# Performance work log

Hardware: AMD Instinct MI355X
Metric: run time of the kernel (lower is better)

Reference implementation:

```python
import jax, jax.numpy as jnp
import numpy as np

B, M, F_IN, DX, K, L, N_ALL = 8192, 10, 128, 128, 64, 32, 100000
NN = M - 1          # n_neigh
INF = float(M)


def layer_norm(x, g, b, eps=1e-5):
    mu = x.mean(-1, keepdims=True)
    var = ((x - mu) ** 2).mean(-1, keepdims=True)
    return (x - mu) * jax.lax.rsqrt(var + eps) * g + b


def bfs_dists(adj, mask):
    # normalized all-pairs hop distances via repeated boolean matmul (m=10 fixed)
    adj_bin = (adj > 1e-5).astype(jnp.float32)
    eye = jnp.eye(M, dtype=bool)
    d = jnp.where(eye[None], 0.0, jnp.where(adj_bin > 0, 1.0, INF))
    curr = adj_bin
    for k in range(2, M):
        curr = jnp.matmul(curr, adj_bin)
        d = jnp.where((curr > 0) & (d == INF), float(k), d)
    mask2 = mask[:, :, None] * mask[:, None, :]
    d = jnp.where(mask2 == 0, INF, d)
    return d / float(M)


def compute_sw(zb, zp, theta, vmask):
    # sliced Wasserstein-2 between batch point clouds [B,NN,d] and prototypes [K,NN,d]
    tn = theta / jnp.linalg.norm(theta, axis=1, keepdims=True)
    pb = jnp.einsum('bmd,ld->bml', zb, tn)
    pp = jnp.einsum('kmd,ld->kml', zp, tn)
    idx = jnp.argsort(pb, axis=1)
    pbs = jnp.take_along_axis(pb, idx, axis=1)
    pps = jnp.sort(pp, axis=1)
    w = jnp.take_along_axis(jnp.broadcast_to(vmask[:, :, None], pb.shape), idx, axis=1)
    w = w / (w.sum(axis=1, keepdims=True) + 1e-9)
    # sum_m w*(pb-pp)^2 expanded to avoid materializing [B,K,NN,L]
    t1 = (w * pbs ** 2).sum(axis=1)                   # [B,L]
    t2 = jnp.einsum('bml,kml->bkl', w * pbs, pps)     # [B,K,L]
    t3 = jnp.einsum('bml,kml->bkl', w, pps ** 2)
    return (t1[:, None, :] - 2.0 * t2 + t3).mean(axis=-1)


def compute_radial(rb, rp, vmask):
    idx = jnp.argsort(rb, axis=1)
    rbs = jnp.take_along_axis(rb, idx, axis=1)
    rps = jnp.sort(rp, axis=1)
    w = jnp.take_along_axis(vmask, idx, axis=1)
    w = w / (w.sum(axis=1, keepdims=True) + 1e-9)
    return (((rbs[:, None, :] - rps[None]) ** 2) * w[:, None, :]).sum(-1)


def setup_inputs() -> dict:
    key = jax.random.key(0)
    ks = jax.random.split(key, 16)
    up = (jax.random.uniform(ks[0], (B, M, M)) < 0.3).astype(jnp.float32)
    adj = jnp.maximum(up, up.transpose(0, 2, 1)) * (1.0 - jnp.eye(M))
    features = jax.random.normal(ks[1], (N_ALL, F_IN), jnp.float32)
    idxs = jax.random.randint(ks[2], (B, M), 0, N_ALL + 1)   # N_ALL == padding index
    rn = lambda k, s, sc=0.02: sc * jax.random.normal(k, s, jnp.float32)
    params = dict(
        x_lin_w=rn(ks[3], (F_IN, DX), 0.05), x_lin_b=jnp.zeros((DX,)),
        x_ln_g=jnp.ones((DX,)), x_ln_b=jnp.zeros((DX,)),
        s_ln_g=jnp.ones((NN,)), s_ln_b=jnp.zeros((NN,)),
        theta_x=jax.random.normal(ks[4], (L, DX), jnp.float32),
        theta_s=jax.random.normal(ks[5], (L, NN), jnp.float32),
        alpha_raw=jnp.zeros(()),
        an_w1=rn(ks[6], (DX, 32), 0.1), an_b1=jnp.zeros((32,)),
        an_w2=rn(ks[7], (32, 1), 0.1), an_b2=jnp.zeros((1,)),
        wn_w1=rn(ks[8], (2 * DX, 32), 0.1), wn_b1=jnp.zeros((32,)),
        wn_w2=rn(ks[9], (32, 1), 0.1), wn_b2=jnp.zeros((1,)),
        w_raw=jnp.zeros(()),
        proto_root=jax.random.normal(ks[10], (K, F_IN), jnp.float32),
        proto_neigh=jax.random.normal(ks[11], (K, NN, F_IN), jnp.float32),
        proto_rad=jax.random.uniform(ks[12], (K, NN)),
        proto_dn=jax.random.uniform(ks[13], (NN * (NN - 1) // 2, K), minval=-0.5, maxval=0.5),
        log_gamma=jnp.asarray(np.log(0.01), jnp.float32),
    )
    return {"adj": adj, "features": features, "idxs": idxs, **params}


def reference(adj, features, idxs, x_lin_w, x_lin_b, x_ln_g, x_ln_b, s_ln_g, s_ln_b,
              theta_x, theta_s, alpha_raw, an_w1, an_b1, an_w2, an_b2,
              wn_w1, wn_b1, wn_w2, wn_b2, w_raw,
              proto_root, proto_neigh, proto_rad, proto_dn, log_gamma):
    b = adj.shape[0]
    x_all = jnp.concatenate([features, jnp.zeros((1, F_IN), features.dtype)], 0)
    x_patch = x_all[idxs]                             # [B,M,F]
    x_root, x_neigh = x_patch[:, 0], x_patch[:, 1:]
    vmask = (idxs[:, 1:] != N_ALL).astype(jnp.float32)   # [B,NN]
    lin = lambda x: x @ x_lin_w + x_lin_b
    h_root = layer_norm(lin(x_root), x_ln_g, x_ln_b)
    h_proto_root = layer_norm(lin(proto_root), x_ln_g, x_ln_b)
    d_root_feat = (jnp.sum(h_root ** 2, -1)[:, None] + jnp.sum(h_proto_root ** 2, -1)[None]
                   - 2.0 * h_root @ h_proto_root.T)   # squared cdist [B,K]
    full_mask = jnp.concatenate([jnp.ones((b, 1), jnp.float32), vmask], 1)
    dists_full = bfs_dists(adj, full_mask)
    d_radial_str = compute_radial(dists_full[:, 0, 1:], proto_rad, vmask)
    h_neigh = layer_norm(lin(x_neigh), x_ln_g, x_ln_b)     # dropout = identity (eval)
    h_proto_neigh = layer_norm(lin(proto_neigh), x_ln_g, x_ln_b)
    sw_neigh_feat = compute_sw(h_neigh, h_proto_neigh, theta_x, vmask)
    hs_neigh = layer_norm(jnp.sort(dists_full[:, 1:, 1:], axis=1), s_ln_g, s_ln_b)
    ti, tj = np.triu_indices(NN, 1)
    C = jnp.zeros((K, NN, NN)).at[:, ti, tj].set(jax.nn.sigmoid(proto_dn).T)
    C = C + C.transpose(0, 2, 1)
    hs_proto = layer_norm(jnp.sort(C, axis=1), s_ln_g, s_ln_b)
    sw_neigh_str = compute_sw(hs_neigh, hs_proto, theta_s, vmask)
    h_pooled = (h_neigh * vmask[:, :, None]).sum(1) / (vmask.sum(1, keepdims=True) + 1e-9)
    alpha_logit = jnp.maximum(h_pooled @ an_w1 + an_b1, 0.0) @ an_w2 + an_b2   # [B,1]
    alpha = jax.nn.sigmoid(alpha_raw + alpha_logit)
    # pairwise w_net([h_root; h_proto_root]) without materializing [B,K,2*DX]
    hb = h_root @ wn_w1[:DX] + wn_b1                   # [B,32]
    hp = h_proto_root @ wn_w1[DX:]                     # [K,32]
    w_logit = (jnp.maximum(hb[:, None] + hp[None], 0.0) @ wn_w2)[..., 0] + wn_b2[0]
    w = jax.nn.sigmoid(w_raw + w_logit)                # [B,K]
    d_feat = w * d_root_feat + (1.0 - w) * sw_neigh_feat
    d_str = w * d_radial_str + (1.0 - w) * sw_neigh_str
    d_fgw = alpha * d_feat + (1.0 - alpha) * d_str
    return jnp.exp(-jnp.exp(log_gamma) * d_fgw)        # [B,K]
```

## Files before the change

### kernel.cpp

```cpp
#include <hip/hip_runtime.h>
#include <hip/hip_bf16.h>

typedef unsigned short u16;
typedef __attribute__((ext_vector_type(8))) short short8;
typedef __attribute__((ext_vector_type(4))) float f32x4;

#define NN 9
#define DX 128
#define KP 64
#define LL 32
#define NALL 100000
#define BMAX 8192
#define NBM 16
#define NBP 64

#define MFMA(a, b, c) __builtin_amdgcn_mfma_f32_16x16x32_bf16(a, b, c, 0, 0, 0)
#define WFENCE() __threadfence_block()

__device__ __align__(16) float g_tns[LL * NN];
__device__ __align__(16) float g_hprn[KP];
__device__ __align__(16) float g_hpt[32 * KP];
__device__ __align__(16) float g_rpst[NN * KP];
__device__ __align__(16) u16   g_hx[BMAX * 10 * DX];
__device__ __align__(16) u16   g_hpool[BMAX * DX];
__device__ __align__(16) float g_hrn[BMAX];
__device__ __align__(16) u16   g_pW[16384];
__device__ __align__(16) u16   g_pBt[4096];
__device__ __align__(16) u16   g_pBr[8192];
__device__ __align__(16) u16   g_pBx[36864];
__device__ __align__(16) u16   g_pBs[36864];
__device__ __align__(16) u16   g_pAn[4096];
__device__ __align__(16) u16   g_pWn[4096];

__device__ __forceinline__ float bf2f(u16 u) {
    union { unsigned u; float f; } v; v.u = ((unsigned)u) << 16; return v.f;
}
__device__ __forceinline__ u16 f2bf(float f) {
    __hip_bfloat16 h = __float2bfloat16(f);
    union { __hip_bfloat16 h; u16 u; } v; v.h = h; return v.u;
}
__device__ __forceinline__ float ldv(const void* p, long i, int f32) {
    return f32 ? ((const float*)p)[i] : bf2f(((const u16*)p)[i]);
}
__device__ __forceinline__ float sigmoidf(float x) { return 1.f / (1.f + expf(-x)); }

__device__ __forceinline__ int bfrag_idx(int ksteps, int ncol, int kd) {
    int ntile = ncol >> 4, n = ncol & 15;
    int kstep = kd >> 5, quad = (kd >> 3) & 3, j = kd & 7;
    return ((ntile * ksteps + kstep) * 64 + quad * 16 + n) * 8 + j;
}

__device__ __forceinline__ void rank9(const float* v, int* r) {
#pragma unroll
    for (int m = 0; m < 9; m++) {
        int rk = 0;
#pragma unroll
        for (int n = 0; n < 9; n++)
            rk += (v[n] < v[m]) || (v[n] == v[m] && n < m);
        r[m] = rk;
    }
}

__global__ __launch_bounds__(256) void k_pack(
    const void* xlw, const void* theta_x, const void* theta_s,
    const void* an_w1, const void* wn_w1, const void* xlg) {
    int t = threadIdx.x;
    const int f32 = (((const u16*)xlg)[0] == 0);
    if (blockIdx.x == 0) {
        for (int i = t; i < 16384; i += 256) {
            int c = i >> 7, d = i & 127;
            g_pW[bfrag_idx(4, d, c)] = f2bf(ldv(xlw, i, f32));
        }
    } else if (blockIdx.x == 1) {
        if (t < 32) {
            float s = 0;
            for (int d = 0; d < 128; d++) { float v = ldv(theta_x, t * 128 + d, f32); s = fmaf(v, v, s); }
            float inv = 1.f / sqrtf(s);
            for (int d = 0; d < 128; d++)
                g_pBt[bfrag_idx(4, t, d)] = f2bf(ldv(theta_x, t * 128 + d, f32) * inv);
        } else if (t < 64) {
            int l = t - 32;
            float s = 0;
            for (int j = 0; j < 9; j++) { float v = ldv(theta_s, l * 9 + j, f32); s = fmaf(v, v, s); }
            float inv = 1.f / sqrtf(s);
            for (int j = 0; j < 9; j++) g_tns[l * 9 + j] = ldv(theta_s, l * 9 + j, f32) * inv;
        }
    } else {
        for (int i = t; i < 4096; i += 256) {
            int d = i >> 5, j = i & 31;
            g_pAn[bfrag_idx(4, j, d)] = f2bf(ldv(an_w1, i, f32));
            g_pWn[bfrag_idx(4, j, d)] = f2bf(ldv(wn_w1, i, f32));
        }
    }
}

__global__ __launch_bounds__(256, 4) void k_lin(
    const void* feat, const int* idxs,
    const void* proto_root, const void* proto_neigh,
    const void* xlb, const void* xlg, const void* xlbt,
    const void* slg, const void* slb, const void* wn_w1,
    const void* proto_rad, const void* proto_dn, int B) {
    __shared__ __align__(16) u16   WfL[16384];
    __shared__ __align__(16) u16   hXpb[1280];
    __shared__ __align__(16) float pbX[288];
    __shared__ __align__(16) float Cm[84];
    __shared__ __align__(16) float hsnP[84];
    u16* hS = WfL;

    int t = threadIdx.x, lane = t & 63, w = t >> 6;
    const int f32 = (((const u16*)xlg)[0] == 0);
    int fm = lane & 15, quad = lane >> 4;
    bool isProto = (blockIdx.x < (unsigned)NBP);
    int rcap = isProto ? 10 : 60;
    int base = isProto ? blockIdx.x * 10 : (blockIdx.x - NBP) * 60;
    int rowT = isProto ? KP * 10 : B * 10;

    {
        const short8* src = (const short8*)g_pW;
        short8* dst = (short8*)WfL;
#pragma unroll
        for (int i = 0; i < 8; i++) dst[t + 256 * i] = src[t + 256 * i];
    }

    int lr = w * 16 + fm, gr = base + lr;
    bool azero = true;
    const void* abuf = feat; long aoff = 0;
    if (lr < rcap && gr < rowT) {
        if (!isProto) {
            int id = idxs[gr];
            if (id != NALL) { azero = false; aoff = (long)id * 128; }
        } else {
            int rr = gr % 10; azero = false;
            if (rr < 9) { abuf = proto_neigh; aoff = (long)((gr / 10) * 9 + rr) * 128; }
            else        { abuf = proto_root;  aoff = (long)(gr / 10) * 128; }
        }
    }
    short8 af[4];
#pragma unroll
    for (int ks = 0; ks < 4; ks++) af[ks] = (short8){0, 0, 0, 0, 0, 0, 0, 0};
    if (!azero) {
        if (f32) {
#pragma unroll
            for (int ks = 0; ks < 4; ks++) {
                const f32x4* src = (const f32x4*)((const float*)abuf + aoff + ks * 32 + quad * 8);
                f32x4 v0 = src[0], v1 = src[1];
                u16* ap = (u16*)&af[ks];
#pragma unroll
                for (int j = 0; j < 4; j++) { ap[j] = f2bf(v0[j]); ap[4 + j] = f2bf(v1[j]); }
            }
        } else {
#pragma unroll
            for (int ks = 0; ks < 4; ks++)
                af[ks] = *(const short8*)((const u16*)abuf + aoff + ks * 32 + quad * 8);
        }
    }
    float bias8[8], gg8[8], bb8[8];
#pragma unroll
    for (int nt = 0; nt < 8; nt++) {
        int col = nt * 16 + fm;
        bias8[nt] = ldv(xlb, col, f32);
        gg8[nt]   = ldv(xlg, col, f32);
        bb8[nt]   = ldv(xlbt, col, f32);
    }
    __syncthreads();

    f32x4 acc[8];
#pragma unroll
    for (int nt = 0; nt < 8; nt++) acc[nt] = (f32x4){0.f, 0.f, 0.f, 0.f};
    if (w * 16 < rcap) {
#pragma unroll
        for (int ks = 0; ks < 4; ks++) {
#pragma unroll
            for (int nt = 0; nt < 8; nt++) {
                short8 bf = *(const short8*)(WfL + ((nt * 4 + ks) * 64 + lane) * 8);
                acc[nt] = MFMA(af[ks], bf, acc[nt]);
            }
        }
    }
    __syncthreads();

    if (w * 16 < rcap) {
#pragma unroll
        for (int reg = 0; reg < 4; reg++) {
            float s = 0, q = 0;
#pragma unroll
            for (int nt = 0; nt < 8; nt++) {
                float v = acc[nt][reg] + bias8[nt];
                s += v; q = fmaf(v, v, q);
            }
#pragma unroll
            for (int m = 1; m < 16; m <<= 1) { s += __shfl_xor(s, m); q += __shfl_xor(q, m); }
            float mu = s * (1.f / 128.f);
            float var = fmaxf(q * (1.f / 128.f) - mu * mu, 0.f);
            float rs = rsqrtf(var + 1e-5f);
            int rowD = w * 16 + quad * 4 + reg, grD = base + rowD;
            if (rowD < rcap && grD < rowT) {
#pragma unroll
                for (int nt = 0; nt < 8; nt++) {
                    float val = (acc[nt][reg] + bias8[nt] - mu) * rs * gg8[nt] + bb8[nt];
                    if (!isProto) hS[rowD * 128 + nt * 16 + fm] = f2bf(val);
                    else          hXpb[rowD * 128 + nt * 16 + fm] = f2bf(val);
                }
            }
        }
    }
    __syncthreads();

    if (!isProto) {
        int nrows = rowT - base; if (nrows > 60) nrows = 60;
        {
            const short8* src = (const short8*)hS;
            short8* dst = (short8*)(g_hx + (long)base * 128);
            for (int i = t; i < nrows * 16; i += 256) dst[i] = src[i];
        }
        if (t < 192) {
            int b = t >> 5, l = t & 31;
            int bg = base / 10 + b;
            if (b * 10 < nrows && bg < B) {
                unsigned msk9 = 0; int cnt = 0;
#pragma unroll
                for (int m = 0; m < 9; m++) {
                    if (idxs[bg * 10 + 1 + m] != NALL) { msk9 |= 1u << m; cnt++; }
                }
                float invb = 1.f / ((float)cnt + 1e-9f);
                float rq = 0;
                unsigned r01, r23;
                {
                    u16 o[4];
#pragma unroll
                    for (int cc = 0; cc < 4; cc++) {
                        int c = l * 4 + cc;
                        float a = 0;
#pragma unroll
                        for (int m = 0; m < 9; m++)
                            if ((msk9 >> m) & 1) a += bf2f(hS[(b * 10 + 1 + m) * 128 + c]);
                        o[cc] = f2bf(a * invb);
                        float rv = bf2f(hS[(b * 10) * 128 + c]);
                        rq = fmaf(rv, rv, rq);
                    }
                    r01 = (unsigned)o[0] | ((unsigned)o[1] << 16);
                    r23 = (unsigned)o[2] | ((unsigned)o[3] << 16);
                }
                unsigned* gp = (unsigned*)(g_hpool + (long)bg * 128);
                gp[l * 2]     = r01;
                gp[l * 2 + 1] = r23;
#pragma unroll
                for (int m = 16; m >= 1; m >>= 1) rq += __shfl_xor(rq, m);
                if (l == 0) g_hrn[bg] = rq;
            }
        }
        return;
    }

    int kb = blockIdx.x;

    for (int i = t; i < 128; i += 256)
        g_pBr[bfrag_idx(4, kb, i)] = hXpb[1152 + i];
    if (w == 0) {
        float v0 = bf2f(hXpb[1152 + lane]);
        float v1 = bf2f(hXpb[1216 + lane]);
        float q = v0 * v0 + v1 * v1;
#pragma unroll
        for (int m = 32; m >= 1; m >>= 1) q += __shfl_xor(q, m);
        if (lane == 0) g_hprn[kb] = q;
    }
    {
        int j = t >> 3, sub = t & 7;
        float a = 0;
#pragma unroll
        for (int dd = 0; dd < 16; dd++) {
            int d = sub * 16 + dd;
            a = fmaf(bf2f(hXpb[1152 + d]), ldv(wn_w1, (128 + d) * 32 + j, f32), a);
        }
        a += __shfl_xor(a, 1);
        a += __shfl_xor(a, 2);
        a += __shfl_xor(a, 4);
        if (sub == 0) g_hpt[j * 64 + kb] = a;
    }
    if (t == 0) {
        float v[9]; int r[9];
#pragma unroll
        for (int m = 0; m < 9; m++) v[m] = ldv(proto_rad, kb * 9 + m, f32);
        rank9(v, r);
#pragma unroll
        for (int m = 0; m < 9; m++) g_rpst[r[m] * 64 + kb] = v[m];
    }
    if (w == 0) {
        f32x4 acc0 = {0.f, 0.f, 0.f, 0.f}, acc1 = {0.f, 0.f, 0.f, 0.f};
        const u16* arow2 = hXpb + fm * 128;
#pragma unroll
        for (int ks = 0; ks < 4; ks++) {
            short8 afp = {0, 0, 0, 0, 0, 0, 0, 0};
            if (fm < 9) afp = *(const short8*)(arow2 + ks * 32 + quad * 8);
            short8 b0 = *(const short8*)(g_pBt + ((0 * 4 + ks) * 64 + lane) * 8);
            short8 b1 = *(const short8*)(g_pBt + ((1 * 4 + ks) * 64 + lane) * 8);
            acc0 = MFMA(afp, b0, acc0);
            acc1 = MFMA(afp, b1, acc1);
        }
#pragma unroll
        for (int reg = 0; reg < 4; reg++) {
            int row = quad * 4 + reg;
            if (row < 9) {
                pbX[row * 32 + fm]      = acc0[reg];
                pbX[row * 32 + 16 + fm] = acc1[reg];
            }
        }
    }
    for (int i = t; i < 81; i += 256) {
        int ii = i / 9, jj = i % 9; float v = 0.f;
        if (ii != jj) {
            int a = (ii < jj) ? ii : jj, b2 = (ii < jj) ? jj : ii;
            int p = a * 8 - a * (a - 1) / 2 + (b2 - a - 1);
            v = sigmoidf(ldv(proto_dn, p * 64 + kb, f32));
        }
        Cm[i] = v;
    }
    __syncthreads();
    if (t < 32) {
        float v[9]; int r[9];
#pragma unroll
        for (int m = 0; m < 9; m++) v[m] = pbX[m * 32 + t];
        rank9(v, r);
#pragma unroll
        for (int m = 0; m < 9; m++) {
            int kd = t * 9 + r[m];
            g_pBx[bfrag_idx(18, kb, kd)]       = f2bf(v[m] * v[m]);
            g_pBx[bfrag_idx(18, kb, 288 + kd)] = f2bf(v[m]);
        }
    }
    if (t >= 64 && t < 73) {
        int col = t - 64;
        float v[9]; int r[9];
#pragma unroll
        for (int j = 0; j < 9; j++) v[j] = Cm[j * 9 + col];
        rank9(v, r);
#pragma unroll
        for (int j = 0; j < 9; j++) Cm[r[j] * 9 + col] = v[j];
    }
    __syncthreads();
    if (t < 9) {
        float mu = 0;
#pragma unroll
        for (int j = 0; j < 9; j++) mu += Cm[t * 9 + j];
        mu *= (1.f / 9.f);
        float var = 0;
#pragma unroll
        for (int j = 0; j < 9; j++) { float d0 = Cm[t * 9 + j] - mu; var = fmaf(d0, d0, var); }
        var *= (1.f / 9.f);
        float rs = rsqrtf(var + 1e-5f);
#pragma unroll
        for (int j = 0; j < 9; j++)
            hsnP[t * 9 + j] = (Cm[t * 9 + j] - mu) * rs * ldv(slg, j, f32) + ldv(slb, j, f32);
    }
    __syncthreads();
    if (t < 32) {
#pragma unroll
        for (int m = 0; m < 9; m++) {
            float a = 0;
#pragma unroll
            for (int j = 0; j < 9; j++) a = fmaf(hsnP[m * 9 + j], g_tns[t * 9 + j], a);
            pbX[m * 32 + t] = a;
        }
    }
    __syncthreads();
    if (t < 32) {
        float v[9]; int r[9];
#pragma unroll
        for (int m = 0; m < 9; m++) v[m] = pbX[m * 32 + t];
        rank9(v, r);
#pragma unroll
        for (int m = 0; m < 9; m++) {
            int kd = t * 9 + r[m];
            g_pBs[bfrag_idx(18, kb, kd)]       = f2bf(v[m] * v[m]);
            g_pBs[bfrag_idx(18, kb, 288 + kd)] = f2bf(v[m]);
        }
    }
}

struct M3 {
    u16   Cf[NBM][584];
    u16   Cs[NBM][584];
    u16   hpoolb[NBM][136];
    float pb[NBM][288];
    float df[NBM][100];
    float hst[NBM][81];
    float drad[NBM][65];
    float hbv[NBM][33];
    float rbss[NBM][9], wrad[NBM][9];
    float sc[NBM][9];
};
__global__ __launch_bounds__(1024, 8) void k_main(
    const void* adj, const int* idxs,
    const void* slg, const void* slb,
    const void* an_b1, const void* an_w2, const void* an_b2,
    const void* wn_b1, const void* wn_w2, const void* wn_b2,
    const void* alpha_raw, const void* w_raw, const void* log_gamma,
    const void* xlg, void* out, int B) {
    __shared__ __align__(16) M3 S;
    int t = threadIdx.x, lane = t & 63, w = t >> 6;
    const int f32 = (((const u16*)xlg)[0] == 0);
    int fm = lane & 15, quad = lane >> 4;
    int bw = blockIdx.x * NBM + w;
    bool bv = (bw < B);

    unsigned long long mb = 0; float nv = 1e-9f, inv = 0.f;

    if (bv) {
        bool valid = false;
        if (lane < 10) {
            int id = idxs[bw * 10 + lane];
            valid = (lane == 0) || (id != NALL);
        }
        mb = __ballot(valid);
        nv = (float)__popcll(mb & 0x3FEull) + 1e-9f;
        inv = 1.f / nv;
        unsigned rowbits = 0;
        if (lane < 10) {
            for (int j = 0; j < 10; j++)
                if (ldv(adj, (long)bw * 100 + lane * 10 + j, f32) > 1e-5f) rowbits |= 1u << j;
        }
        int dl[10];
#pragma unroll
        for (int j = 0; j < 10; j++) dl[j] = (j == lane) ? 0 : (((rowbits >> j) & 1) ? 1 : 10);
        unsigned reach = (lane < 10) ? (rowbits | (1u << lane)) : 0u;
        for (int s = 2; s <= 9; s++) {
            unsigned nr = reach;
#pragma unroll
            for (int j = 0; j < 10; j++) {
                unsigned rj = __shfl(rowbits, j);
                if ((reach >> j) & 1) nr |= rj;
            }
            unsigned add = nr & ~reach;
#pragma unroll
            for (int j = 0; j < 10; j++) if ((add >> j) & 1) dl[j] = s;
            reach = nr;
            if (__all(add == 0)) break;
        }
        if (lane < 10) {
            int mi = (int)((mb >> lane) & 1);
#pragma unroll
            for (int j = 0; j < 10; j++) {
                int mj = (int)((mb >> j) & 1);
                S.df[w][lane * 10 + j] = (mi && mj) ? (float)dl[j] * 0.1f : 1.0f;
            }
        }
        {
            float v[9];
#pragma unroll
            for (int m = 0; m < 9; m++) {
                float vm = ((mb >> (1 + m)) & 1) ? (float)dl[1 + m] * 0.1f : 1.0f;
                v[m] = __shfl(vm, 0);
            }
            if (lane < 9) {
                float mine = v[0];
#pragma unroll
                for (int m = 1; m < 9; m++) if (lane == m) mine = v[m];
                int rk = 0;
#pragma unroll
                for (int n = 0; n < 9; n++) rk += (v[n] < mine) || (v[n] == mine && n < lane);
                S.rbss[w][rk] = mine;
                S.wrad[w][rk] = (((mb >> (1 + lane)) & 1) ? 1.f : 0.f) * inv;
            }
        }
        if (lane == 0) S.sc[w][1] = g_hrn[bw];
        ((unsigned*)S.hpoolb[w])[lane] = ((const unsigned*)(g_hpool + (long)bw * 128))[lane];
        {
            f32x4 acc0 = {0.f, 0.f, 0.f, 0.f}, acc1 = {0.f, 0.f, 0.f, 0.f};
            const u16* arow = g_hx + (bw * 10 + 1 + fm) * 128;
#pragma unroll
            for (int ks = 0; ks < 4; ks++) {
                short8 af = {0, 0, 0, 0, 0, 0, 0, 0};
                if (fm < 9) af = *(const short8*)(arow + ks * 32 + quad * 8);
                short8 b0 = *(const short8*)(g_pBt + ((0 * 4 + ks) * 64 + lane) * 8);
                short8 b1 = *(const short8*)(g_pBt + ((1 * 4 + ks) * 64 + lane) * 8);
                acc0 = MFMA(af, b0, acc0);
                acc1 = MFMA(af, b1, acc1);
            }
#pragma unroll
            for (int reg = 0; reg < 4; reg++) {
                int row = quad * 4 + reg;
                if (row < 9) {
                    S.pb[w][row * 32 + fm]      = acc0[reg];
                    S.pb[w][row * 32 + 16 + fm] = acc1[reg];
                }
            }
        }
        WFENCE();

        {
            float t1 = 0;
            if (lane < 32) {
                float v[9]; int r[9];
#pragma unroll
                for (int m = 0; m < 9; m++) v[m] = S.pb[w][m * 32 + lane];
                rank9(v, r);
#pragma unroll
                for (int m = 0; m < 9; m++) {
                    float wgt = (((mb >> (1 + m)) & 1) ? 1.f : 0.f) * inv;
                    int slot = lane * 9 + r[m];
                    S.Cf[w][slot]       = f2bf(wgt);
                    S.Cf[w][288 + slot] = f2bf(-2.f * wgt * v[m]);
                    t1 = fmaf(wgt * v[m], v[m], t1);
                }
            }
#pragma unroll
            for (int m = 16; m >= 1; m >>= 1) t1 += __shfl_xor(t1, m);
            if (lane == 0) S.sc[w][3] = t1;
        }
        if (lane < 9) {
            float v[9]; int r[9];
#pragma unroll
            for (int i = 0; i < 9; i++) v[i] = S.df[w][(1 + i) * 10 + 1 + lane];
            rank9(v, r);
#pragma unroll
            for (int i = 0; i < 9; i++) S.hst[w][r[i] * 9 + lane] = v[i];
        }
        {
            float acc = 0;
#pragma unroll
            for (int m = 0; m < 9; m++) {
                float d0 = S.rbss[w][m] - g_rpst[m * 64 + lane];
                acc = fmaf(d0 * d0, S.wrad[w][m], acc);
            }
            S.drad[w][lane] = acc;
        }
        WFENCE();

        if (lane < 9) {
            float vv[9];
#pragma unroll
            for (int j = 0; j < 9; j++) vv[j] = S.hst[w][lane * 9 + j];
            float mu = 0;
#pragma unroll
            for (int j = 0; j < 9; j++) mu += vv[j];
            mu *= (1.f / 9.f);
            float var = 0;
#pragma unroll
            for (int j = 0; j < 9; j++) { float d0 = vv[j] - mu; var = fmaf(d0, d0, var); }
            var *= (1.f / 9.f);
            float rs = rsqrtf(var + 1e-5f);
#pragma unroll
            for (int j = 0; j < 9; j++)
                S.hst[w][lane * 9 + j] = (vv[j] - mu) * rs * ldv(slg, j, f32) + ldv(slb, j, f32);
        }
        WFENCE();

        {
            int l = lane & 31;
            int m0 = (lane < 32) ? 0 : 5, m1 = (lane < 32) ? 5 : 9;
            for (int m = m0; m < m1; m++) {
                float a = 0;
#pragma unroll
                for (int j = 0; j < 9; j++) a = fmaf(S.hst[w][m * 9 + j], g_tns[l * 9 + j], a);
                S.pb[w][m * 32 + l] = a;
            }
        }
        WFENCE();

        {
            float t1 = 0;
            if (lane < 32) {
                float v[9]; int r[9];
#pragma unroll
                for (int m = 0; m < 9; m++) v[m] = S.pb[w][m * 32 + lane];
                rank9(v, r);
#pragma unroll
                for (int m = 0; m < 9; m++) {
                    float wgt = (((mb >> (1 + m)) & 1) ? 1.f : 0.f) * inv;
                    int slot = lane * 9 + r[m];
                    S.Cs[w][slot]       = f2bf(wgt);
                    S.Cs[w][288 + slot] = f2bf(-2.f * wgt * v[m]);
                    t1 = fmaf(wgt * v[m], v[m], t1);
                }
            }
#pragma unroll
            for (int m = 16; m >= 1; m >>= 1) t1 += __shfl_xor(t1, m);
            if (lane == 0) S.sc[w][4] = t1;
        }
    }
    __syncthreads();

    f32x4 rd = {0.f, 0.f, 0.f, 0.f};
    f32x4 accF = {0.f, 0.f, 0.f, 0.f}, accS = {0.f, 0.f, 0.f, 0.f};
    if (w < 4) {
#pragma unroll
        for (int ks = 0; ks < 4; ks++) {
            short8 af = {0, 0, 0, 0, 0, 0, 0, 0};
            int bb = blockIdx.x * NBM + fm;
            if (bb < B) af = *(const short8*)(g_hx + (long)bb * 1280 + ks * 32 + quad * 8);
            short8 bfr = *(const short8*)(g_pBr + ((w * 4 + ks) * 64 + lane) * 8);
            rd = MFMA(af, bfr, rd);
        }
#pragma unroll
        for (int ks = 0; ks < 18; ks++) {
            short8 aF = *(const short8*)(S.Cf[fm] + ks * 32 + quad * 8);
            short8 aS = *(const short8*)(S.Cs[fm] + ks * 32 + quad * 8);
            short8 bF = *(const short8*)(g_pBx + ((w * 18 + ks) * 64 + lane) * 8);
            short8 bS = *(const short8*)(g_pBs + ((w * 18 + ks) * 64 + lane) * 8);
            accF = MFMA(aF, bF, accF);
            accS = MFMA(aS, bS, accS);
        }
    } else if (w == 4) {
        f32x4 a0 = {0.f, 0.f, 0.f, 0.f}, a1 = {0.f, 0.f, 0.f, 0.f};
#pragma unroll
        for (int ks = 0; ks < 4; ks++) {
            short8 af = {0, 0, 0, 0, 0, 0, 0, 0};
            int bb = blockIdx.x * NBM + fm;
            if (bb < B) af = *(const short8*)(g_hx + (long)bb * 1280 + ks * 32 + quad * 8);
            short8 b0 = *(const short8*)(g_pWn + ((0 * 4 + ks) * 64 + lane) * 8);
            short8 b1 = *(const short8*)(g_pWn + ((1 * 4 + ks) * 64 + lane) * 8);
            a0 = MFMA(af, b0, a0);
            a1 = MFMA(af, b1, a1);
        }
        float wb0 = ldv(wn_b1, fm, f32), wb1 = ldv(wn_b1, 16 + fm, f32);
#pragma unroll
        for (int reg = 0; reg < 4; reg++) {
            int b = quad * 4 + reg;
            S.hbv[b][fm]      = a0[reg] + wb0;
            S.hbv[b][16 + fm] = a1[reg] + wb1;
        }
    } else if (w == 5) {
        f32x4 a0 = {0.f, 0.f, 0.f, 0.f}, a1 = {0.f, 0.f, 0.f, 0.f};
#pragma unroll
        for (int ks = 0; ks < 4; ks++) {
            short8 af = *(const short8*)(S.hpoolb[fm] + ks * 32 + quad * 8);
            short8 b0 = *(const short8*)(g_pAn + ((0 * 4 + ks) * 64 + lane) * 8);
            short8 b1 = *(const short8*)(g_pAn + ((1 * 4 + ks) * 64 + lane) * 8);
            a0 = MFMA(af, b0, a0);
            a1 = MFMA(af, b1, a1);
        }
        float ab0 = ldv(an_b1, fm, f32), ab1 = ldv(an_b1, 16 + fm, f32);
        float aw0 = ldv(an_w2, fm, f32), aw1 = ldv(an_w2, 16 + fm, f32);
        float araw = ldv(alpha_raw, 0, f32), ab2 = ldv(an_b2, 0, f32);
#pragma unroll
        for (int reg = 0; reg < 4; reg++) {
            float s = fmaxf(a0[reg] + ab0, 0.f) * aw0 + fmaxf(a1[reg] + ab1, 0.f) * aw1;
            s += __shfl_xor(s, 1); s += __shfl_xor(s, 2);
            s += __shfl_xor(s, 4); s += __shfl_xor(s, 8);
            if (fm == 0) S.sc[quad * 4 + reg][2] = sigmoidf(araw + s + ab2);
        }
    }
    __syncthreads();

    if (w < 4) {
        int k = w * 16 + fm;
        float wb2 = ldv(wn_b2, 0, f32);
        float wr  = ldv(w_raw, 0, f32);
        float gamma = expf(ldv(log_gamma, 0, f32));
        float hprnk = g_hprn[k];
        float wl[4] = {0.f, 0.f, 0.f, 0.f};
#pragma unroll 4
        for (int j = 0; j < 32; j++) {
            float hptv = g_hpt[j * 64 + k];
            float w2v = ldv(wn_w2, j, f32);
#pragma unroll
            for (int reg = 0; reg < 4; reg++)
                wl[reg] = fmaf(fmaxf(S.hbv[quad * 4 + reg][j] + hptv, 0.f), w2v, wl[reg]);
        }
#pragma unroll
        for (int reg = 0; reg < 4; reg++) {
            int b = quad * 4 + reg, bb = blockIdx.x * NBM + b;
            if (bb >= B) continue;
            float swf = (S.sc[b][3] + accF[reg]) * (1.f / 32.f);
            float sws = (S.sc[b][4] + accS[reg]) * (1.f / 32.f);
            float drfk = S.sc[b][1] + hprnk - 2.f * rd[reg];
            float wgt = sigmoidf(wr + wl[reg] + wb2);
            float dfeat = wgt * drfk + (1.f - wgt) * swf;
            float dstr  = wgt * S.drad[b][k] + (1.f - wgt) * sws;
            float al = S.sc[b][2];
            float dfgw = al * dfeat + (1.f - al) * dstr;
            if (!(dfgw == dfgw)) dfgw = 1e30f;
            float res = expf(-gamma * dfgw);
            if (f32) ((float*)out)[(long)bb * 64 + k] = res;
            else     ((u16*)out)[(long)bb * 64 + k] = f2bf(res);
        }
    }
}

extern "C" void kernel_launch(void* const* d_in, const int* in_sizes, int n_in,
                              void* d_out, int out_size, void* d_ws, size_t ws_size,
                              hipStream_t stream) {
    const void* adj  = d_in[0];
    const void* feat = d_in[1];
    const int*  idxs = (const int*)d_in[2];
    const void* xlw  = d_in[3];
    const void* xlb  = d_in[4];
    const void* xlg  = d_in[5];
    const void* xlbt = d_in[6];
    const void* slg  = d_in[7];
    const void* slb  = d_in[8];
    const void* thx  = d_in[9];
    const void* ths  = d_in[10];
    const void* araw = d_in[11];
    const void* anw1 = d_in[12];
    const void* anb1 = d_in[13];
    const void* anw2 = d_in[14];
    const void* anb2 = d_in[15];
    const void* wnw1 = d_in[16];
    const void* wnb1 = d_in[17];
    const void* wnw2 = d_in[18];
    const void* wnb2 = d_in[19];
    const void* wraw = d_in[20];
    const void* prt  = d_in[21];
    const void* prn  = d_in[22];
    const void* prad = d_in[23];
    const void* pdn  = d_in[24];
    const void* lgam = d_in[25];
    int B = in_sizes[2] / 10;
    int NBQ = (B * 10 + 59) / 60;

    k_pack<<<3, 256, 0, stream>>>(xlw, thx, ths, anw1, wnw1, xlg);
    k_lin<<<NBP + NBQ, 256, 0, stream>>>(feat, idxs, prt, prn,
                                         xlb, xlg, xlbt, slg, slb, wnw1,
                                         prad, pdn, B);
    k_main<<<(B + NBM - 1) / NBM, 1024, 0, stream>>>(adj, idxs, slg, slb,
                                  anb1, anw2, anb2, wnb1, wnw2, wnb2,
                                  araw, wraw, lgam, xlg, d_out, B);
}
```

Before: 211.8 us.

## Move per-sample BFS, sorting and projection prep from k_main into k_lin

The per-sample preprocessing (BFS hop distances, neighbour projections onto theta_x, rank sorting, structural layer norm, theta_s projection, radial distances) moves out of k_main and into the k_lin epilogue. There it runs on the hidden states already in shared memory, so the full 10-row hidden tensor is no longer written to and reread from global memory. k_lin now writes compact per-sample buffers (Cf/Cs coefficient matrices, t1 terms, radial distances, the root row), which k_main just loads before its MFMA stage. Prototype radial sorting moves into k_pack. The cost is extra global buffers and more serial, lightly parallel work with extra barriers in k_lin.

After: 216.2 us. 1.02x slower.

```diff
diff --git a/kernel.cpp b/kernel.cpp
--- a/kernel.cpp
+++ b/kernel.cpp
@@ -15,15 +15,19 @@
 #define NBP 64
 
 #define MFMA(a, b, c) __builtin_amdgcn_mfma_f32_16x16x32_bf16(a, b, c, 0, 0, 0)
-#define WFENCE() __threadfence_block()
 
 __device__ __align__(16) float g_tns[LL * NN];
 __device__ __align__(16) float g_hprn[KP];
 __device__ __align__(16) float g_hpt[32 * KP];
 __device__ __align__(16) float g_rpst[NN * KP];
-__device__ __align__(16) u16   g_hx[BMAX * 10 * DX];
+__device__ __align__(16) u16   g_hroot[BMAX * DX];
 __device__ __align__(16) u16   g_hpool[BMAX * DX];
 __device__ __align__(16) float g_hrn[BMAX];
+__device__ __align__(16) u16   g_Cf[BMAX * 576];
+__device__ __align__(16) u16   g_Cs[BMAX * 576];
+__device__ __align__(16) float g_drad[BMAX * 64];
+__device__ __align__(16) float g_t1x[BMAX];
+__device__ __align__(16) float g_t1s[BMAX];
 __device__ __align__(16) u16   g_pW[16384];
 __device__ __align__(16) u16   g_pBt[4096];
 __device__ __align__(16) u16   g_pBr[8192];
@@ -63,7 +67,7 @@
 
 __global__ __launch_bounds__(256) void k_pack(
     const void* xlw, const void* theta_x, const void* theta_s,
-    const void* an_w1, const void* wn_w1, const void* xlg) {
+    const void* an_w1, const void* wn_w1, const void* proto_rad, const void* xlg) {
     int t = threadIdx.x;
     const int f32 = (((const u16*)xlg)[0] == 0);
     if (blockIdx.x == 0) {
@@ -84,6 +88,14 @@
             for (int j = 0; j < 9; j++) { float v = ldv(theta_s, l * 9 + j, f32); s = fmaf(v, v, s); }
             float inv = 1.f / sqrtf(s);
             for (int j = 0; j < 9; j++) g_tns[l * 9 + j] = ldv(theta_s, l * 9 + j, f32) * inv;
+        } else if (t < 128) {
+            int k = t - 64;
+            float v[9]; int r[9];
+#pragma unroll
+            for (int m = 0; m < 9; m++) v[m] = ldv(proto_rad, k * 9 + m, f32);
+            rank9(v, r);
+#pragma unroll
+            for (int m = 0; m < 9; m++) g_rpst[r[m] * 64 + k] = v[m];
         }
     } else {
         for (int i = t; i < 4096; i += 256) {
@@ -95,17 +107,24 @@
 }
 
 __global__ __launch_bounds__(256, 4) void k_lin(
-    const void* feat, const int* idxs,
+    const void* adj, const void* feat, const int* idxs,
     const void* proto_root, const void* proto_neigh,
     const void* xlb, const void* xlg, const void* xlbt,
     const void* slg, const void* slb, const void* wn_w1,
-    const void* proto_rad, const void* proto_dn, int B) {
+    const void* proto_dn, int B) {
     __shared__ __align__(16) u16   WfL[16384];
     __shared__ __align__(16) u16   hXpb[1280];
     __shared__ __align__(16) float pbX[288];
     __shared__ __align__(16) float Cm[84];
     __shared__ __align__(16) float hsnP[84];
-    u16* hS = WfL;
+    u16*      hS    = WfL;
+    float*    dfL   = (float*)((char*)WfL + 15360);
+    float*    stL   = (float*)((char*)WfL + 17760);
+    float*    pbU   = (float*)((char*)WfL + 19712);
+    float*    rbssL = (float*)((char*)WfL + 26624);
+    float*    wradL = (float*)((char*)WfL + 26840);
+    unsigned* gmL   = (unsigned*)((char*)WfL + 27056);
+    float*    invL  = (float*)((char*)WfL + 27080);
 
     int t = threadIdx.x, lane = t & 63, w = t >> 6;
     const int f32 = (((const u16*)xlg)[0] == 0);
@@ -114,6 +133,7 @@
     int rcap = isProto ? 10 : 60;
     int base = isProto ? blockIdx.x * 10 : (blockIdx.x - NBP) * 60;
     int rowT = isProto ? KP * 10 : B * 10;
+    int bbase = base / 10;
 
     {
         const short8* src = (const short8*)g_pW;
@@ -208,15 +228,77 @@
 
     if (!isProto) {
         int nrows = rowT - base; if (nrows > 60) nrows = 60;
-        {
-            const short8* src = (const short8*)hS;
-            short8* dst = (short8*)(g_hx + (long)base * 128);
-            for (int i = t; i < nrows * 16; i += 256) dst[i] = src[i];
+        int nb = nrows / 10;
+
+        if (w < 2) {
+            int g2 = lane >> 4, b = w * 4 + g2, j = lane & 15, srcb = lane & 48;
+            bool bact = (b < nb);
+            int bg = bbase + b;
+            bool vj = false;
+            if (bact && j < 10) vj = (j == 0) || (idxs[bg * 10 + j] != NALL);
+            unsigned long long bal = __ballot(vj);
+            unsigned gm = (unsigned)(bal >> srcb) & 0x3FFu;
+            float invb = 1.f / ((float)__popc(gm & 0x3FEu) + 1e-9f);
+            unsigned rowbits = 0;
+            if (bact && j < 10) {
+                for (int jj = 0; jj < 10; jj++)
+                    if (ldv(adj, (long)bg * 100 + j * 10 + jj, f32) > 1e-5f) rowbits |= 1u << jj;
+            }
+            int dl[10];
+#pragma unroll
+            for (int jj = 0; jj < 10; jj++) dl[jj] = (jj == j) ? 0 : (((rowbits >> jj) & 1) ? 1 : 10);
+            unsigned reach = (j < 10) ? (rowbits | (1u << j)) : 0u;
+            for (int s = 2; s <= 9; s++) {
+                unsigned nr = reach;
+#pragma unroll
+                for (int jj = 0; jj < 10; jj++) {
+                    unsigned rj = (unsigned)__shfl((int)rowbits, srcb + jj);
+                    if ((reach >> jj) & 1) nr |= rj;
+                }
+                unsigned add = nr & ~reach;
+#pragma unroll
+                for (int jj = 0; jj < 10; jj++) if ((add >> jj) & 1) dl[jj] = s;
+                reach = nr;
+                if (__all(add == 0)) break;
+            }
+            if (bact && j < 10) {
+                int mi = (int)((gm >> j) & 1);
+#pragma unroll
+                for (int jj = 0; jj < 10; jj++) {
+                    int mj = (int)((gm >> jj) & 1);
+                    dfL[b * 100 + j * 10 + jj] = (mi && mj) ? (float)dl[jj] * 0.1f : 1.0f;
+                }
+            }
+            {
+                float v[9];
+#pragma unroll
+                for (int m = 0; m < 9; m++) {
+                    int dv = __shfl(dl[1 + m], srcb);
+                    v[m] = ((gm >> (1 + m)) & 1) ? (float)dv * 0.1f : 1.0f;
+                }
+                if (bact && j < 9) {
+                    float mine = v[0];
+#pragma unroll
+                    for (int m = 1; m < 9; m++) if (j == m) mine = v[m];
+                    int rk = 0;
+#pragma unroll
+                    for (int n = 0; n < 9; n++) rk += (v[n] < mine) || (v[n] == mine && n < j);
+                    rbssL[b * 9 + rk] = mine;
+                    wradL[b * 9 + rk] = (((gm >> (1 + j)) & 1) ? 1.f : 0.f) * invb;
+                }
+                if (bact && j == 0) { gmL[b] = gm; invL[b] = invb; }
+            }
+        }
+
+        if (t < 96) {
+            int b = t >> 4, i = t & 15;
+            if (b < nb)
+                ((short8*)(g_hroot + (long)(bbase + b) * 128))[i] = ((const short8*)(hS + b * 10 * 128))[i];
         }
         if (t < 192) {
             int b = t >> 5, l = t & 31;
-            int bg = base / 10 + b;
-            if (b * 10 < nrows && bg < B) {
+            int bg = bbase + b;
+            if (b < nb) {
                 unsigned msk9 = 0; int cnt = 0;
 #pragma unroll
                 for (int m = 0; m < 9; m++) {
@@ -224,30 +306,157 @@
                 }
                 float invb = 1.f / ((float)cnt + 1e-9f);
                 float rq = 0;
-                unsigned r01, r23;
-                {
-                    u16 o[4];
-#pragma unroll
-                    for (int cc = 0; cc < 4; cc++) {
-                        int c = l * 4 + cc;
-                        float a = 0;
-#pragma unroll
-                        for (int m = 0; m < 9; m++)
-                            if ((msk9 >> m) & 1) a += bf2f(hS[(b * 10 + 1 + m) * 128 + c]);
-                        o[cc] = f2bf(a * invb);
-                        float rv = bf2f(hS[(b * 10) * 128 + c]);
-                        rq = fmaf(rv, rv, rq);
-                    }
-                    r01 = (unsigned)o[0] | ((unsigned)o[1] << 16);
-                    r23 = (unsigned)o[2] | ((unsigned)o[3] << 16);
+                u16 o[4];
+#pragma unroll
+                for (int cc = 0; cc < 4; cc++) {
+                    int c = l * 4 + cc;
+                    float a = 0;
+#pragma unroll
+                    for (int m = 0; m < 9; m++)
+                        if ((msk9 >> m) & 1) a += bf2f(hS[(b * 10 + 1 + m) * 128 + c]);
+                    o[cc] = f2bf(a * invb);
+                    float rv = bf2f(hS[(b * 10) * 128 + c]);
+                    rq = fmaf(rv, rv, rq);
                 }
                 unsigned* gp = (unsigned*)(g_hpool + (long)bg * 128);
-                gp[l * 2]     = r01;
-                gp[l * 2 + 1] = r23;
+                gp[l * 2]     = (unsigned)o[0] | ((unsigned)o[1] << 16);
+                gp[l * 2 + 1] = (unsigned)o[2] | ((unsigned)o[3] << 16);
 #pragma unroll
                 for (int m = 16; m >= 1; m >>= 1) rq += __shfl_xor(rq, m);
                 if (l == 0) g_hrn[bg] = rq;
             }
+        }
+
+        {
+            f32x4 acc0 = {0.f, 0.f, 0.f, 0.f}, acc1 = {0.f, 0.f, 0.f, 0.f};
+            int row = w * 16 + fm;
+            bool act = (row < nrows) && (row % 10 != 0);
+            const u16* arow = hS + row * 128;
+#pragma unroll
+            for (int ks = 0; ks < 4; ks++) {
+                short8 afn = {0, 0, 0, 0, 0, 0, 0, 0};
+                if (act) afn = *(const short8*)(arow + ks * 32 + quad * 8);
+                short8 b0 = *(const short8*)(g_pBt + ((0 * 4 + ks) * 64 + lane) * 8);
+                short8 b1 = *(const short8*)(g_pBt + ((1 * 4 + ks) * 64 + lane) * 8);
+                acc0 = MFMA(afn, b0, acc0);
+                acc1 = MFMA(afn, b1, acc1);
+            }
+#pragma unroll
+            for (int reg = 0; reg < 4; reg++) {
+                int rowD = w * 16 + quad * 4 + reg;
+                if (rowD < nrows && (rowD % 10) != 0) {
+                    int b = rowD / 10, m = rowD % 10 - 1;
+                    pbU[b * 288 + m * 32 + fm]      = acc0[reg];
+                    pbU[b * 288 + m * 32 + 16 + fm] = acc1[reg];
+                }
+            }
+        }
+        __syncthreads();
+
+        if (t < 192) {
+            int b = t >> 5, l = t & 31;
+            if (b < nb) {
+                int bg = bbase + b;
+                unsigned gm = gmL[b]; float invb = invL[b];
+                float v[9]; int r[9];
+#pragma unroll
+                for (int m = 0; m < 9; m++) v[m] = pbU[b * 288 + m * 32 + l];
+                rank9(v, r);
+                float t1 = 0;
+#pragma unroll
+                for (int m = 0; m < 9; m++) {
+                    float wgt = (((gm >> (1 + m)) & 1) ? 1.f : 0.f) * invb;
+                    int slot = l * 9 + r[m];
+                    g_Cf[(long)bg * 576 + slot]       = f2bf(wgt);
+                    g_Cf[(long)bg * 576 + 288 + slot] = f2bf(-2.f * wgt * v[m]);
+                    t1 = fmaf(wgt * v[m], v[m], t1);
+                }
+#pragma unroll
+                for (int m = 16; m >= 1; m >>= 1) t1 += __shfl_xor(t1, m);
+                if (l == 0) g_t1x[bg] = t1;
+            }
+        }
+        if (t < 54) {
+            int b = t / 9, col = t - b * 9;
+            if (b < nb) {
+                float v[9]; int r[9];
+#pragma unroll
+                for (int i = 0; i < 9; i++) v[i] = dfL[b * 100 + (1 + i) * 10 + 1 + col];
+                rank9(v, r);
+#pragma unroll
+                for (int i = 0; i < 9; i++) stL[b * 81 + r[i] * 9 + col] = v[i];
+            }
+        }
+        __syncthreads();
+
+        if (t < 54) {
+            int b = t / 9, row = t - b * 9;
+            if (b < nb) {
+                float vv[9];
+#pragma unroll
+                for (int j = 0; j < 9; j++) vv[j] = stL[b * 81 + row * 9 + j];
+                float mu = 0;
+#pragma unroll
+                for (int j = 0; j < 9; j++) mu += vv[j];
+                mu *= (1.f / 9.f);
+                float var = 0;
+#pragma unroll
+                for (int j = 0; j < 9; j++) { float d0 = vv[j] - mu; var = fmaf(d0, d0, var); }
+                var *= (1.f / 9.f);
+                float rs = rsqrtf(var + 1e-5f);
+#pragma unroll
+                for (int j = 0; j < 9; j++)
+                    stL[b * 81 + row * 9 + j] = (vv[j] - mu) * rs * ldv(slg, j, f32) + ldv(slb, j, f32);
+            }
+        }
+        __syncthreads();
+
+        if (t < 192) {
+            int b = t >> 5, l = t & 31;
+            if (b < nb) {
+#pragma unroll
+                for (int m = 0; m < 9; m++) {
+                    float a = 0;
+#pragma unroll
+                    for (int j = 0; j < 9; j++) a = fmaf(stL[b * 81 + m * 9 + j], g_tns[l * 9 + j], a);
+                    pbU[b * 288 + m * 32 + l] = a;
+                }
+            }
+        }
+        __syncthreads();
+
+        if (t < 192) {
+            int b = t >> 5, l = t & 31;
+            if (b < nb) {
+                int bg = bbase + b;
+                unsigned gm = gmL[b]; float invb = invL[b];
+                float v[9]; int r[9];
+#pragma unroll
+                for (int m = 0; m < 9; m++) v[m] = pbU[b * 288 + m * 32 + l];
+                rank9(v, r);
+                float t1 = 0;
+#pragma unroll
+                for (int m = 0; m < 9; m++) {
+                    float wgt = (((gm >> (1 + m)) & 1) ? 1.f : 0.f) * invb;
+                    int slot = l * 9 + r[m];
+                    g_Cs[(long)bg * 576 + slot]       = f2bf(wgt);
+                    g_Cs[(long)bg * 576 + 288 + slot] = f2bf(-2.f * wgt * v[m]);
+                    t1 = fmaf(wgt * v[m], v[m], t1);
+                }
+#pragma unroll
+                for (int m = 16; m >= 1; m >>= 1) t1 += __shfl_xor(t1, m);
+                if (l == 0) g_t1s[bg] = t1;
+            }
+        }
+        for (int i = t; i < nb * 64; i += 256) {
+            int b = i >> 6, k = i & 63;
+            float a = 0;
+#pragma unroll
+            for (int m = 0; m < 9; m++) {
+                float d0 = rbssL[b * 9 + m] - g_rpst[m * 64 + k];
+                a = fmaf(d0 * d0, wradL[b * 9 + m], a);
+            }
+            g_drad[(long)(bbase + b) * 64 + k] = a;
         }
         return;
     }
@@ -276,14 +485,6 @@
         a += __shfl_xor(a, 2);
         a += __shfl_xor(a, 4);
         if (sub == 0) g_hpt[j * 64 + kb] = a;
-    }
-    if (t == 0) {
-        float v[9]; int r[9];
-#pragma unroll
-        for (int m = 0; m < 9; m++) v[m] = ldv(proto_rad, kb * 9 + m, f32);
-        rank9(v, r);
-#pragma unroll
-        for (int m = 0; m < 9; m++) g_rpst[r[m] * 64 + kb] = v[m];
     }
     if (w == 0) {
         f32x4 acc0 = {0.f, 0.f, 0.f, 0.f}, acc1 = {0.f, 0.f, 0.f, 0.f};
@@ -380,18 +581,13 @@
 struct M3 {
     u16   Cf[NBM][584];
     u16   Cs[NBM][584];
+    u16   hrootL[NBM][136];
     u16   hpoolb[NBM][136];
-    float pb[NBM][288];
-    float df[NBM][100];
-    float hst[NBM][81];
     float drad[NBM][65];
     float hbv[NBM][33];
-    float rbss[NBM][9], wrad[NBM][9];
     float sc[NBM][9];
 };
 __global__ __launch_bounds__(1024, 8) void k_main(
-    const void* adj, const int* idxs,
-    const void* slg, const void* slb,
     const void* an_b1, const void* an_w2, const void* an_b2,
     const void* wn_b1, const void* wn_w2, const void* wn_b2,
     const void* alpha_raw, const void* w_raw, const void* log_gamma,
@@ -403,179 +599,36 @@
     int bw = blockIdx.x * NBM + w;
     bool bv = (bw < B);
 
-    unsigned long long mb = 0; float nv = 1e-9f, inv = 0.f;
-
     if (bv) {
-        bool valid = false;
-        if (lane < 10) {
-            int id = idxs[bw * 10 + lane];
-            valid = (lane == 0) || (id != NALL);
-        }
-        mb = __ballot(valid);
-        nv = (float)__popcll(mb & 0x3FEull) + 1e-9f;
-        inv = 1.f / nv;
-        unsigned rowbits = 0;
-        if (lane < 10) {
-            for (int j = 0; j < 10; j++)
-                if (ldv(adj, (long)bw * 100 + lane * 10 + j, f32) > 1e-5f) rowbits |= 1u << j;
-        }
-        int dl[10];
-#pragma unroll
-        for (int j = 0; j < 10; j++) dl[j] = (j == lane) ? 0 : (((rowbits >> j) & 1) ? 1 : 10);
-        unsigned reach = (lane < 10) ? (rowbits | (1u << lane)) : 0u;
-        for (int s = 2; s <= 9; s++) {
-            unsigned nr = reach;
-#pragma unroll
-            for (int j = 0; j < 10; j++) {
-                unsigned rj = __shfl(rowbits, j);
-                if ((reach >> j) & 1) nr |= rj;
-            }
-            unsigned add = nr & ~reach;
-#pragma unroll
-            for (int j = 0; j < 10; j++) if ((add >> j) & 1) dl[j] = s;
-            reach = nr;
-            if (__all(add == 0)) break;
-        }
-        if (lane < 10) {
-            int mi = (int)((mb >> lane) & 1);
-#pragma unroll
-            for (int j = 0; j < 10; j++) {
-                int mj = (int)((mb >> j) & 1);
-                S.df[w][lane * 10 + j] = (mi && mj) ? (float)dl[j] * 0.1f : 1.0f;
-            }
-        }
         {
-            float v[9];
-#pragma unroll
-            for (int m = 0; m < 9; m++) {
-                float vm = ((mb >> (1 + m)) & 1) ? (float)dl[1 + m] * 0.1f : 1.0f;
-                v[m] = __shfl(vm, 0);
-            }
-            if (lane < 9) {
-                float mine = v[0];
-#pragma unroll
-                for (int m = 1; m < 9; m++) if (lane == m) mine = v[m];
-                int rk = 0;
-#pragma unroll
-                for (int n = 0; n < 9; n++) rk += (v[n] < mine) || (v[n] == mine && n < lane);
-                S.rbss[w][rk] = mine;
-                S.wrad[w][rk] = (((mb >> (1 + lane)) & 1) ? 1.f : 0.f) * inv;
-            }
-        }
-        if (lane == 0) S.sc[w][1] = g_hrn[bw];
-        ((unsigned*)S.hpoolb[w])[lane] = ((const unsigned*)(g_hpool + (long)bw * 128))[lane];
+            const short8* src = (const short8*)(g_Cf + (long)bw * 576);
+            short8* dst = (short8*)S.Cf[w];
+            for (int i = lane; i < 72; i += 64) dst[i] = src[i];
+        }
         {
-            f32x4 acc0 = {0.f, 0.f, 0.f, 0.f}, acc1 = {0.f, 0.f, 0.f, 0.f};
-            const u16* arow = g_hx + (bw * 10 + 1 + fm) * 128;
-#pragma unroll
-            for (int ks = 0; ks < 4; ks++) {
-                short8 af = {0, 0, 0, 0, 0, 0, 0, 0};
-                if (fm < 9) af = *(const short8*)(arow + ks * 32 + quad * 8);
-                short8 b0 = *(const short8*)(g_pBt + ((0 * 4 + ks) * 64 + lane) * 8);
-                short8 b1 = *(const short8*)(g_pBt + ((1 * 4 + ks) * 64 + lane) * 8);
-                acc0 = MFMA(af, b0, acc0);
-                acc1 = MFMA(af, b1, acc1);
-            }
-#pragma unroll
-            for (int reg = 0; reg < 4; reg++) {
-                int row = quad * 4 + reg;
-                if (row < 9) {
-                    S.pb[w][row * 32 + fm]      = acc0[reg];
-                    S.pb[w][row * 32 + 16 + fm] = acc1[reg];
-                }
-            }
-        }
-        WFENCE();
-
-        {
-            float t1 = 0;
-            if (lane < 32) {
-                float v[9]; int r[9];
-#pragma unroll
-                for (int m = 0; m < 9; m++) v[m] = S.pb[w][m * 32 + lane];
-                rank9(v, r);
-#pragma unroll
-                for (int m = 0; m < 9; m++) {
-                    float wgt = (((mb >> (1 + m)) & 1) ? 1.f : 0.f) * inv;
-                    int slot = lane * 9 + r[m];
-                    S.Cf[w][slot]       = f2bf(wgt);
-                    S.Cf[w][288 + slot] = f2bf(-2.f * wgt * v[m]);
-                    t1 = fmaf(wgt * v[m], v[m], t1);
-                }
-            }
-#pragma unroll
-            for (int m = 16; m >= 1; m >>= 1) t1 += __shfl_xor(t1, m);
-            if (lane == 0) S.sc[w][3] = t1;
-        }
-        if (lane < 9) {
-            float v[9]; int r[9];
-#pragma unroll
-            for (int i = 0; i < 9; i++) v[i] = S.df[w][(1 + i) * 10 + 1 + lane];
-            rank9(v, r);
-#pragma unroll
-            for (int i = 0; i < 9; i++) S.hst[w][r[i] * 9 + lane] = v[i];
-        }
-        {
-            float acc = 0;
-#pragma unroll
-            for (int m = 0; m < 9; m++) {
-                float d0 = S.rbss[w][m] - g_rpst[m * 64 + lane];
-                acc = fmaf(d0 * d0, S.wrad[w][m], acc);
-            }
-            S.drad[w][lane] = acc;
-        }
-        WFENCE();
-
-        if (lane < 9) {
-            float vv[9];
-#pragma unroll
-            for (int j = 0; j < 9; j++) vv[j] = S.hst[w][lane * 9 + j];
-            float mu = 0;
-#pragma unroll
-            for (int j = 0; j < 9; j++) mu += vv[j];
-            mu *= (1.f / 9.f);
-            float var = 0;
-#pragma unroll
-            for (int j = 0; j < 9; j++) { float d0 = vv[j] - mu; var = fmaf(d0, d0, var); }
-            var *= (1.f / 9.f);
-            float rs = rsqrtf(var + 1e-5f);
-#pragma unroll
-            for (int j = 0; j < 9; j++)
-                S.hst[w][lane * 9 + j] = (vv[j] - mu) * rs * ldv(slg, j, f32) + ldv(slb, j, f32);
-        }
-        WFENCE();
-
-        {
-            int l = lane & 31;
-            int m0 = (lane < 32) ? 0 : 5, m1 = (lane < 32) ? 5 : 9;
-            for (int m = m0; m < m1; m++) {
-                float a = 0;
-#pragma unroll
-                for (int j = 0; j < 9; j++) a = fmaf(S.hst[w][m * 9 + j], g_tns[l * 9 + j], a);
-                S.pb[w][m * 32 + l] = a;
-            }
-        }
-        WFENCE();
-
-        {
-            float t1 = 0;
-            if (lane < 32) {
-                float v[9]; int r[9];
-#pragma unroll
-                for (int m = 0; m < 9; m++) v[m] = S.pb[w][m * 32 + lane];
-                rank9(v, r);
-#pragma unroll
-                for (int m = 0; m < 9; m++) {
-                    float wgt = (((mb >> (1 + m)) & 1) ? 1.f : 0.f) * inv;
-                    int slot = lane * 9 + r[m];
-                    S.Cs[w][slot]       = f2bf(wgt);
-                    S.Cs[w][288 + slot] = f2bf(-2.f * wgt * v[m]);
-                    t1 = fmaf(wgt * v[m], v[m], t1);
-                }
-            }
-#pragma unroll
-            for (int m = 16; m >= 1; m >>= 1) t1 += __shfl_xor(t1, m);
-            if (lane == 0) S.sc[w][4] = t1;
+            const short8* src = (const short8*)(g_Cs + (long)bw * 576);
+            short8* dst = (short8*)S.Cs[w];
+            for (int i = lane; i < 72; i += 64) dst[i] = src[i];
+        }
+        if (lane < 16) {
+            ((short8*)S.hrootL[w])[lane] = ((const short8*)(g_hroot + (long)bw * 128))[lane];
+            ((short8*)S.hpoolb[w])[lane] = ((const short8*)(g_hpool + (long)bw * 128))[lane];
+        }
+        S.drad[w][lane] = g_drad[(long)bw * 64 + lane];
+        if (lane == 0) {
+            S.sc[w][1] = g_hrn[bw];
+            S.sc[w][3] = g_t1x[bw];
+            S.sc[w][4] = g_t1s[bw];
+        }
+    } else {
+        short8 z = {0, 0, 0, 0, 0, 0, 0, 0};
+        for (int i = lane; i < 72; i += 64) {
+            ((short8*)S.Cf[w])[i] = z;
+            ((short8*)S.Cs[w])[i] = z;
+        }
+        if (lane < 16) {
+            ((short8*)S.hrootL[w])[lane] = z;
+            ((short8*)S.hpoolb[w])[lane] = z;
         }
     }
     __syncthreads();
@@ -585,9 +638,7 @@
     if (w < 4) {
 #pragma unroll
         for (int ks = 0; ks < 4; ks++) {
-            short8 af = {0, 0, 0, 0, 0, 0, 0, 0};
-            int bb = blockIdx.x * NBM + fm;
-            if (bb < B) af = *(const short8*)(g_hx + (long)bb * 1280 + ks * 32 + quad * 8);
+            short8 af = *(const short8*)(S.hrootL[fm] + ks * 32 + quad * 8);
             short8 bfr = *(const short8*)(g_pBr + ((w * 4 + ks) * 64 + lane) * 8);
             rd = MFMA(af, bfr, rd);
         }
@@ -604,9 +655,7 @@
         f32x4 a0 = {0.f, 0.f, 0.f, 0.f}, a1 = {0.f, 0.f, 0.f, 0.f};
 #pragma unroll
         for (int ks = 0; ks < 4; ks++) {
-            short8 af = {0, 0, 0, 0, 0, 0, 0, 0};
-            int bb = blockIdx.x * NBM + fm;
-            if (bb < B) af = *(const short8*)(g_hx + (long)bb * 1280 + ks * 32 + quad * 8);
+            short8 af = *(const short8*)(S.hrootL[fm] + ks * 32 + quad * 8);
             short8 b0 = *(const short8*)(g_pWn + ((0 * 4 + ks) * 64 + lane) * 8);
             short8 b1 = *(const short8*)(g_pWn + ((1 * 4 + ks) * 64 + lane) * 8);
             a0 = MFMA(af, b0, a0);
@@ -709,11 +758,11 @@
     int B = in_sizes[2] / 10;
     int NBQ = (B * 10 + 59) / 60;
 
-    k_pack<<<3, 256, 0, stream>>>(xlw, thx, ths, anw1, wnw1, xlg);
-    k_lin<<<NBP + NBQ, 256, 0, stream>>>(feat, idxs, prt, prn,
+    k_pack<<<3, 256, 0, stream>>>(xlw, thx, ths, anw1, wnw1, prad, xlg);
+    k_lin<<<NBP + NBQ, 256, 0, stream>>>(adj, feat, idxs, prt, prn,
                                          xlb, xlg, xlbt, slg, slb, wnw1,
-                                         prad, pdn, B);
-    k_main<<<(B + NBM - 1) / NBM, 1024, 0, stream>>>(adj, idxs, slg, slb,
+                                         pdn, B);
+    k_main<<<(B + NBM - 1) / NBM, 1024, 0, stream>>>(
                                   anb1, anw2, anb2, wnb1, wnw2, wnb2,
                                   araw, wraw, lgam, xlg, d_out, B);
 }
```
